# Kernel optimization log

Hardware: AMD Instinct MI355X
Metric: run time of the kernel (lower is better)

The kernel has to match this reference:

```python
import jax, jax.numpy as jnp
import numpy as np

N_TX = 1_000_000   # transaction nodes
N_W  = 250_000     # wallet nodes
E    = 2_000_000   # edges per relation
F_TX, F_W = 64, 32 # raw feature dims
H, OUT = 64, 2     # hidden, out (module defaults)


def setup_inputs() -> dict:
    key = jax.random.key(0)
    ks = jax.random.split(key, 40)
    f32 = jnp.float32
    def w(i, shape):
        return jax.random.normal(ks[i], shape, dtype=f32) * 0.05
    inp = {}
    inp["x_tx"] = jax.random.normal(ks[0], (N_TX, F_TX), dtype=f32)
    inp["x_w"]  = jax.random.normal(ks[1], (N_W, F_W), dtype=f32)
    inp["src_tw"] = jax.random.randint(ks[2], (E,), 0, N_TX)
    inp["dst_tw"] = jax.random.randint(ks[3], (E,), 0, N_W)
    inp["src_wt"] = jax.random.randint(ks[4], (E,), 0, N_W)
    inp["dst_wt"] = jax.random.randint(ks[5], (E,), 0, N_TX)
    # lin_in per node type
    inp["Win_tx"], inp["bin_tx"] = w(6, (F_TX, H)), w(7, (H,))
    inp["Win_w"],  inp["bin_w"]  = w(8, (F_W, H)),  w(9, (H,))
    # conv1: SAGEConv per edge type (lin_l has bias, lin_r no bias)
    inp["Wl1_tw"], inp["bl1_tw"], inp["Wr1_tw"] = w(10, (H, H)), w(11, (H,)), w(12, (H, H))
    inp["Wl1_wt"], inp["bl1_wt"], inp["Wr1_wt"] = w(13, (H, H)), w(14, (H,)), w(15, (H, H))
    # conv2
    inp["Wl2_tw"], inp["bl2_tw"], inp["Wr2_tw"] = w(16, (H, H)), w(17, (H,)), w(18, (H, H))
    inp["Wl2_wt"], inp["bl2_wt"], inp["Wr2_wt"] = w(19, (H, H)), w(20, (H,)), w(21, (H, H))
    # tx head
    inp["Wh1"], inp["bh1"] = w(22, (H, H)), w(23, (H,))
    inp["Wh2"], inp["bh2"] = w(24, (H, OUT)), w(25, (OUT,))
    return inp


def _sage(x_src, x_dst, src, dst, Wl, bl, Wr, n_dst):
    # PyG SAGEConv: lin_l(mean_{j->i} x_src[j]) + lin_r(x_dst[i])
    agg = jax.ops.segment_sum(x_src[src], dst, num_segments=n_dst)
    cnt = jax.ops.segment_sum(jnp.ones((src.shape[0],), x_src.dtype), dst,
                              num_segments=n_dst)
    mean = agg / jnp.maximum(cnt, 1.0)[:, None]
    return mean @ Wl + bl + x_dst @ Wr


def reference(x_tx, x_w, src_tw, dst_tw, src_wt, dst_wt,
              Win_tx, bin_tx, Win_w, bin_w,
              Wl1_tw, bl1_tw, Wr1_tw, Wl1_wt, bl1_wt, Wr1_wt,
              Wl2_tw, bl2_tw, Wr2_tw, Wl2_wt, bl2_wt, Wr2_wt,
              Wh1, bh1, Wh2, bh2):
    # per-type input projection
    h_tx = x_tx @ Win_tx + bin_tx   # [N_TX, H]
    h_w  = x_w @ Win_w + bin_w      # [N_W, H]
    # conv1 (HeteroConv aggr='sum'; each dst type has one relation) + relu
    w1 = jax.nn.relu(_sage(h_tx, h_w,  src_tw, dst_tw, Wl1_tw, bl1_tw, Wr1_tw, N_W))
    t1 = jax.nn.relu(_sage(h_w,  h_tx, src_wt, dst_wt, Wl1_wt, bl1_wt, Wr1_wt, N_TX))
    # conv2 + relu
    w2 = jax.nn.relu(_sage(t1, w1, src_tw, dst_tw, Wl2_tw, bl2_tw, Wr2_tw, N_W))
    t2 = jax.nn.relu(_sage(w1, t1, src_wt, dst_wt, Wl2_wt, bl2_wt, Wr2_wt, N_TX))
    # tx head (dropout inactive in eval)
    logits = jax.nn.relu(t2 @ Wh1 + bh1) @ Wh2 + bh2  # [N_TX, 2]
    return (logits, t2, w2)
```

## Files before the change

### kernel.cpp

```cpp
#include <hip/hip_runtime.h>
#include <hip/hip_bf16.h>

typedef __hip_bfloat16 bf16;
typedef __attribute__((ext_vector_type(8))) short bf16x8;
typedef __attribute__((ext_vector_type(4))) float f32x4;

__device__ __forceinline__ float b2f(bf16 v) { return __bfloat162float(v); }
__device__ __forceinline__ bf16 f2b(float v) { return __float2bfloat16(v); }
__device__ __forceinline__ unsigned short f2bb(float v) {
    unsigned int u = __float_as_uint(v);
    u += 0x7fffu + ((u >> 16) & 1u);
    return (unsigned short)(u >> 16);
}
__device__ __forceinline__ float b2fx(bf16x8 v, int k) {
    return __uint_as_float(((unsigned int)(unsigned short)v[k]) << 16);
}

__device__ __forceinline__ f32x4 mfma16(bf16x8 a, bf16x8 b, f32x4 c) {
    return __builtin_amdgcn_mfma_f32_16x16x32_bf16(a, b, c, 0, 0, 0);
}

__device__ __forceinline__ bf16x8 load_bfrag(const float* __restrict__ W, int k0, int col) {
    bf16x8 f;
#pragma unroll
    for (int j = 0; j < 8; ++j)
        f[j] = (short)f2bb(W[(size_t)(k0 + j) * 64 + col]);
    return f;
}

__device__ __forceinline__ int swzH(int row, int b) {
    return row * 128 + (b ^ ((row & 7) << 4));
}

__global__ void count_rank2_kernel(const int* __restrict__ dst_tw, int* __restrict__ deg_w,
                                   int* __restrict__ rank_tw, int ne_tw,
                                   const int* __restrict__ dst_wt, int* __restrict__ deg_tx,
                                   int* __restrict__ rank_wt, int ne_wt) {
    int e = blockIdx.x * 256 + threadIdx.x;
    if (e < ne_tw) rank_tw[e] = atomicAdd(&deg_w[dst_tw[e]], 1);
    else {
        int e2 = e - ne_tw;
        if (e2 < ne_wt) rank_wt[e2] = atomicAdd(&deg_tx[dst_wt[e2]], 1);
    }
}

__global__ void scan1m_kernel(const int* __restrict__ dw, int* __restrict__ ew,
                              int* __restrict__ pw, int nw, int npw,
                              const int* __restrict__ dt, int* __restrict__ et,
                              int* __restrict__ pt, int nt) {
    __shared__ int sT[256];
    const int* deg; int* excl; int* partial; int n; int b;
    if ((int)blockIdx.x < npw) { deg = dw; excl = ew; partial = pw; n = nw; b = blockIdx.x; }
    else { deg = dt; excl = et; partial = pt; n = nt; b = blockIdx.x - npw; }
    int tid = threadIdx.x;
    int base = b * 1024 + tid * 4;
    int v0 = (base + 0 < n) ? deg[base + 0] : 0;
    int v1 = (base + 1 < n) ? deg[base + 1] : 0;
    int v2 = (base + 2 < n) ? deg[base + 2] : 0;
    int v3 = (base + 3 < n) ? deg[base + 3] : 0;
    int t = v0 + v1 + v2 + v3;
    sT[tid] = t;
    __syncthreads();
    for (int off = 1; off < 256; off <<= 1) {
        int x = (tid >= off) ? sT[tid - off] : 0;
        __syncthreads();
        sT[tid] += x;
        __syncthreads();
    }
    int et2 = sT[tid] - t;
    if (tid == 255) partial[b] = sT[255];
    if (base + 0 < n) excl[base + 0] = et2;
    if (base + 1 < n) excl[base + 1] = et2 + v0;
    if (base + 2 < n) excl[base + 2] = et2 + v0 + v1;
    if (base + 3 < n) excl[base + 3] = et2 + v0 + v1 + v2;
}

__global__ void scan2m_kernel(int* __restrict__ pw, int npw, int* __restrict__ pt, int npt) {
    __shared__ int sT[256];
    __shared__ int carry;
    int* partial = blockIdx.x ? pt : pw;
    int np = blockIdx.x ? npt : npw;
    int tid = threadIdx.x;
    if (tid == 0) carry = 0;
    __syncthreads();
    for (int c = 0; c < np; c += 256) {
        int i = c + tid;
        int v = (i < np) ? partial[i] : 0;
        sT[tid] = v;
        __syncthreads();
        for (int off = 1; off < 256; off <<= 1) {
            int x = (tid >= off) ? sT[tid - off] : 0;
            __syncthreads();
            sT[tid] += x;
            __syncthreads();
        }
        int incl = sT[tid];
        int total = sT[255];
        if (i < np) partial[i] = carry + incl - v;
        __syncthreads();
        if (tid == 0) carry += total;
        __syncthreads();
    }
}

__global__ void scan3m_kernel(const int* __restrict__ ew, const int* __restrict__ pw,
                              int* __restrict__ rw, int nw, int nbw,
                              const int* __restrict__ et, const int* __restrict__ pt,
                              int* __restrict__ rt, int nt) {
    int b = blockIdx.x;
    const int* excl; const int* partial; int* rp; int n; int i;
    if (b < nbw) { i = b * 256 + threadIdx.x; excl = ew; partial = pw; rp = rw; n = nw; }
    else { i = (b - nbw) * 256 + threadIdx.x; excl = et; partial = pt; rp = rt; n = nt; }
    if (i < n) rp[i] = excl[i] + partial[i >> 10];
}

__device__ __forceinline__ void proj64_body(const float* __restrict__ x,
                                            const float* __restrict__ W,
                                            const float* __restrict__ b,
                                            bf16* __restrict__ out, int n, int bid) {
    int tid = threadIdx.x;
    int lane = tid & 63, w = tid >> 6;
    int lm = lane & 15, lq = lane >> 4;

    bf16x8 wc[4][2];
    float bv[4];
#pragma unroll
    for (int ct = 0; ct < 4; ++ct) {
        int colc = ct * 16 + lm;
        wc[ct][0] = load_bfrag(W, lq * 8, colc);
        wc[ct][1] = load_bfrag(W, 32 + lq * 8, colc);
        bv[ct] = b[colc];
    }

    int larow = w * 16 + lm;
    int row0 = bid * 512;
    if (row0 >= n) return;
    int ar = row0 + larow; ar = (ar < n) ? ar : (n - 1);
    const float* xrow = x + ((size_t)ar << 6);
    float4 p0 = *(const float4*)(xrow + lq * 8);
    float4 p1 = *(const float4*)(xrow + lq * 8 + 4);
    float4 p2 = *(const float4*)(xrow + 32 + lq * 8);
    float4 p3 = *(const float4*)(xrow + 32 + lq * 8 + 4);

    for (int g = 0; g < 8; ++g) {
        int gr0 = row0 + g * 64;
        if (gr0 >= n) break;
        float4 q0 = p0, q1 = p1, q2 = p2, q3 = p3;
        if (g < 7) {
            int nr = gr0 + 64 + larow; nr = (nr < n) ? nr : (n - 1);
            const float* nx = x + ((size_t)nr << 6);
            q0 = *(const float4*)(nx + lq * 8);
            q1 = *(const float4*)(nx + lq * 8 + 4);
            q2 = *(const float4*)(nx + 32 + lq * 8);
            q3 = *(const float4*)(nx + 32 + lq * 8 + 4);
        }
        bf16x8 a0, a1;
        a0[0] = (short)f2bb(p0.x); a0[1] = (short)f2bb(p0.y);
        a0[2] = (short)f2bb(p0.z); a0[3] = (short)f2bb(p0.w);
        a0[4] = (short)f2bb(p1.x); a0[5] = (short)f2bb(p1.y);
        a0[6] = (short)f2bb(p1.z); a0[7] = (short)f2bb(p1.w);
        a1[0] = (short)f2bb(p2.x); a1[1] = (short)f2bb(p2.y);
        a1[2] = (short)f2bb(p2.z); a1[3] = (short)f2bb(p2.w);
        a1[4] = (short)f2bb(p3.x); a1[5] = (short)f2bb(p3.y);
        a1[6] = (short)f2bb(p3.z); a1[7] = (short)f2bb(p3.w);
#pragma unroll
        for (int ct = 0; ct < 4; ++ct) {
            f32x4 acc = {0.f, 0.f, 0.f, 0.f};
            acc = mfma16(a0, wc[ct][0], acc);
            acc = mfma16(a1, wc[ct][1], acc);
            int colc = ct * 16 + lm;
#pragma unroll
            for (int r = 0; r < 4; ++r) {
                int grow = gr0 + w * 16 + lq * 4 + r;
                if (grow < n)
                    out[(size_t)grow * 64 + colc] = f2b(acc[r] + bv[ct]);
            }
        }
        p0 = q0; p1 = q1; p2 = q2; p3 = q3;
    }
}

__device__ __forceinline__ void proj32_body(const float* __restrict__ x,
                                            const float* __restrict__ W,
                                            const float* __restrict__ b,
                                            bf16* __restrict__ out, int n, int bid,
                                            float (*sW)[64], float* sb, float (*sx)[32]) {
    const int F = 32;
    int tid = threadIdx.x;
    for (int idx = tid; idx < F * 16; idx += 256)
        ((float4*)sW)[idx] = ((const float4*)W)[idx];
    if (tid < 64) sb[tid] = b[tid];
    int base = bid * 64;
    int w = tid >> 6, j = tid & 63;
    int lw = w * 4;
    for (int g = 0; g < 4; ++g) {
        int row0 = base + g * 16;
        __syncthreads();
        for (int idx = tid; idx < 4 * F; idx += 256) {
            int rr = idx / (F / 4), c4 = idx - rr * (F / 4);
            int row = row0 + rr;
            float4 v = (row < n) ? ((const float4*)x)[(size_t)row * (F / 4) + c4]
                                 : make_float4(0.f, 0.f, 0.f, 0.f);
            *(float4*)&sx[rr][c4 * 4] = v;
        }
        __syncthreads();
        float a0 = sb[j], a1 = sb[j], a2 = sb[j], a3 = sb[j];
#pragma unroll 2
        for (int k = 0; k < F; k += 4) {
            float w0 = sW[k][j], w1 = sW[k + 1][j], w2 = sW[k + 2][j], w3 = sW[k + 3][j];
            float4 m0 = *(const float4*)&sx[lw + 0][k];
            float4 m1 = *(const float4*)&sx[lw + 1][k];
            float4 m2 = *(const float4*)&sx[lw + 2][k];
            float4 m3 = *(const float4*)&sx[lw + 3][k];
            a0 += m0.x * w0 + m0.y * w1 + m0.z * w2 + m0.w * w3;
            a1 += m1.x * w0 + m1.y * w1 + m1.z * w2 + m1.w * w3;
            a2 += m2.x * w0 + m2.y * w1 + m2.z * w2 + m2.w * w3;
            a3 += m3.x * w0 + m3.y * w1 + m3.z * w2 + m3.w * w3;
        }
        int r0 = row0 + lw;
        if (r0 + 0 < n) out[(size_t)(r0 + 0) * 64 + j] = f2b(a0);
        if (r0 + 1 < n) out[(size_t)(r0 + 1) * 64 + j] = f2b(a1);
        if (r0 + 2 < n) out[(size_t)(r0 + 2) * 64 + j] = f2b(a2);
        if (r0 + 3 < n) out[(size_t)(r0 + 3) * 64 + j] = f2b(a3);
    }
}

__global__ __launch_bounds__(256)
void fused_front_kernel(const int* __restrict__ src_tw, const int* __restrict__ dst_tw,
                        const int* __restrict__ rank_tw, const int* __restrict__ rp_w,
                        int* __restrict__ col_tw, int ne_tw,
                        const int* __restrict__ src_wt, const int* __restrict__ dst_wt,
                        const int* __restrict__ rank_wt, const int* __restrict__ rp_tx,
                        int* __restrict__ col_wt, int ne_wt, int gsc,
                        const float* __restrict__ x_tx, const float* __restrict__ Win_tx,
                        const float* __restrict__ bin_tx, bf16* __restrict__ A, int n_tx, int gp64,
                        const float* __restrict__ x_w, const float* __restrict__ Win_w,
                        const float* __restrict__ bin_w, bf16* __restrict__ B, int n_w) {
    __shared__ float sW32[32][64];
    __shared__ float sb32[64];
    __shared__ float sx32[16][32];
    int bid = blockIdx.x;
    if (bid < gsc) {
        int e = bid * 256 + threadIdx.x;
        if (e < ne_tw) {
            col_tw[rp_w[dst_tw[e]] + rank_tw[e]] = src_tw[e];
        } else {
            int e2 = e - ne_tw;
            if (e2 < ne_wt)
                col_wt[rp_tx[dst_wt[e2]] + rank_wt[e2]] = src_wt[e2];
        }
    } else if (bid < gsc + gp64) {
        proj64_body(x_tx, Win_tx, bin_tx, A, n_tx, bid - gsc);
    } else {
        proj32_body(x_w, Win_w, bin_w, B, n_w, bid - gsc - gp64, sW32, sb32, sx32);
    }
}

#define GA4(x, wt) \
    p0 += (wt) * b2fx(x, 0); p1 += (wt) * b2fx(x, 1); \
    p2 += (wt) * b2fx(x, 2); p3 += (wt) * b2fx(x, 3); \
    p4 += (wt) * b2fx(x, 4); p5 += (wt) * b2fx(x, 5); \
    p6 += (wt) * b2fx(x, 6); p7 += (wt) * b2fx(x, 7);
#define GB4(x, wt) \
    q0 += (wt) * b2fx(x, 0); q1 += (wt) * b2fx(x, 1); \
    q2 += (wt) * b2fx(x, 2); q3 += (wt) * b2fx(x, 3); \
    q4 += (wt) * b2fx(x, 4); q5 += (wt) * b2fx(x, 5); \
    q6 += (wt) * b2fx(x, 6); q7 += (wt) * b2fx(x, 7);

template<bool HEAD>
__device__ __forceinline__ void sageg_body(
        const bf16* __restrict__ hsrc, const int* __restrict__ rowptr,
        const int* __restrict__ deg, const int* __restrict__ col,
        const bf16* __restrict__ xd,
        const float* __restrict__ Wl, const float* __restrict__ bl,
        const float* __restrict__ Wr,
        float* __restrict__ outf, bf16* __restrict__ outb,
        const float* __restrict__ Wh1, const float* __restrict__ bh1,
        const float* __restrict__ Wh2, const float* __restrict__ bh2,
        float* __restrict__ logits, int n, int bid, short* sH) {
    int tid = threadIdx.x;
    int lane = tid & 63, w = tid >> 6;
    int lm = lane & 15, lq = lane >> 4;

    bf16x8 wc[4][4];
    bf16x8 wh[4][2];
    float blv[4], h1v[4], w2a[4], w2b[4];
#pragma unroll
    for (int ct = 0; ct < 4; ++ct) {
        int colc = ct * 16 + lm;
        wc[ct][0] = load_bfrag(Wl, lq * 8, colc);
        wc[ct][1] = load_bfrag(Wl, 32 + lq * 8, colc);
        wc[ct][2] = load_bfrag(Wr, lq * 8, colc);
        wc[ct][3] = load_bfrag(Wr, 32 + lq * 8, colc);
        blv[ct] = bl[colc];
        if (HEAD) {
            wh[ct][0] = load_bfrag(Wh1, lq * 8, colc);
            wh[ct][1] = load_bfrag(Wh1, 32 + lq * 8, colc);
            h1v[ct] = bh1[colc];
            w2a[ct] = Wh2[colc * 2 + 0];
            w2b[ct] = Wh2[colc * 2 + 1];
        }
    }
    float b20 = 0.f, b21 = 0.f;
    if (HEAD) { b20 = bh2[0]; b21 = bh2[1]; }

    int larow = w * 16 + lm;
    int row0 = bid * 512;
    if (row0 >= n) return;
    int fo1 = lq * 8, fo2 = 32 + lq * 8;

    for (int g = 0; g < 8; ++g) {
        int gr0 = row0 + g * 64;
        if (gr0 >= n) break;
        int arow = gr0 + larow;
        int ar = (arow < n) ? arow : (n - 1);
        const bf16* xrow = xd + ((size_t)ar << 6);
        bf16x8 a2 = *(const bf16x8*)(xrow + fo1);
        bf16x8 a3 = *(const bf16x8*)(xrow + fo2);
        int base = rowptr[ar];
        int d = deg[ar];
        int lasto = (d > 0) ? d - 1 : 0;
        float p0 = 0.f, p1 = 0.f, p2 = 0.f, p3 = 0.f;
        float p4 = 0.f, p5 = 0.f, p6 = 0.f, p7 = 0.f;
        float q0 = 0.f, q1 = 0.f, q2 = 0.f, q3 = 0.f;
        float q4 = 0.f, q5 = 0.f, q6 = 0.f, q7 = 0.f;
        for (int e0 = 0; e0 < d; e0 += 4) {
            int o1 = (e0 + 1 < d) ? e0 + 1 : lasto;
            int o2 = (e0 + 2 < d) ? e0 + 2 : lasto;
            int o3 = (e0 + 3 < d) ? e0 + 3 : lasto;
            int s0 = col[base + e0], s1 = col[base + o1];
            int s2 = col[base + o2], s3 = col[base + o3];
            const bf16* r0p = hsrc + ((size_t)s0 << 6);
            const bf16* r1p = hsrc + ((size_t)s1 << 6);
            const bf16* r2p = hsrc + ((size_t)s2 << 6);
            const bf16* r3p = hsrc + ((size_t)s3 << 6);
            bf16x8 xa0 = *(const bf16x8*)(r0p + fo1);
            bf16x8 xb0 = *(const bf16x8*)(r0p + fo2);
            bf16x8 xa1 = *(const bf16x8*)(r1p + fo1);
            bf16x8 xb1 = *(const bf16x8*)(r1p + fo2);
            bf16x8 xa2 = *(const bf16x8*)(r2p + fo1);
            bf16x8 xb2 = *(const bf16x8*)(r2p + fo2);
            bf16x8 xa3 = *(const bf16x8*)(r3p + fo1);
            bf16x8 xb3 = *(const bf16x8*)(r3p + fo2);
            float w1 = (e0 + 1 < d) ? 1.f : 0.f;
            float w2 = (e0 + 2 < d) ? 1.f : 0.f;
            float w3 = (e0 + 3 < d) ? 1.f : 0.f;
            GA4(xa0, 1.f) GB4(xb0, 1.f)
            GA4(xa1, w1)  GB4(xb1, w1)
            GA4(xa2, w2)  GB4(xb2, w2)
            GA4(xa3, w3)  GB4(xb3, w3)
        }
        float dd = fmaxf((float)d, 1.f);
        bf16x8 a0, a1;
        a0[0] = (short)f2bb(p0 / dd); a0[1] = (short)f2bb(p1 / dd);
        a0[2] = (short)f2bb(p2 / dd); a0[3] = (short)f2bb(p3 / dd);
        a0[4] = (short)f2bb(p4 / dd); a0[5] = (short)f2bb(p5 / dd);
        a0[6] = (short)f2bb(p6 / dd); a0[7] = (short)f2bb(p7 / dd);
        a1[0] = (short)f2bb(q0 / dd); a1[1] = (short)f2bb(q1 / dd);
        a1[2] = (short)f2bb(q2 / dd); a1[3] = (short)f2bb(q3 / dd);
        a1[4] = (short)f2bb(q4 / dd); a1[5] = (short)f2bb(q5 / dd);
        a1[6] = (short)f2bb(q6 / dd); a1[7] = (short)f2bb(q7 / dd);

#pragma unroll
        for (int ct = 0; ct < 4; ++ct) {
            f32x4 acc = {0.f, 0.f, 0.f, 0.f};
            acc = mfma16(a0, wc[ct][0], acc);
            acc = mfma16(a1, wc[ct][1], acc);
            acc = mfma16(a2, wc[ct][2], acc);
            acc = mfma16(a3, wc[ct][3], acc);
            int colc = ct * 16 + lm;
#pragma unroll
            for (int r = 0; r < 4; ++r) {
                int lrow = w * 16 + lq * 4 + r;
                int grow = gr0 + lrow;
                float v = fmaxf(acc[r] + blv[ct], 0.f);
                if (grow < n) {
                    if (outf) outf[(size_t)grow * 64 + colc] = v;
                    if (outb) outb[(size_t)grow * 64 + colc] = f2b(v);
                }
                if (HEAD)
                    *(short*)((char*)sH + swzH(lrow, colc * 2)) = (short)f2bb(v);
            }
        }
        if (HEAD) {
            bf16x8 h0 = *(const bf16x8*)((char*)sH + swzH(larow, lq * 16));
            bf16x8 h1 = *(const bf16x8*)((char*)sH + swzH(larow, 64 + lq * 16));
            float qa0 = 0.f, qa1 = 0.f, qa2 = 0.f, qa3 = 0.f;
            float qb0 = 0.f, qb1 = 0.f, qb2 = 0.f, qb3 = 0.f;
#pragma unroll
            for (int ct = 0; ct < 4; ++ct) {
                f32x4 acc = {0.f, 0.f, 0.f, 0.f};
                acc = mfma16(h0, wh[ct][0], acc);
                acc = mfma16(h1, wh[ct][1], acc);
                float hb = h1v[ct];
                float h_0 = fmaxf(acc[0] + hb, 0.f);
                float h_1 = fmaxf(acc[1] + hb, 0.f);
                float h_2 = fmaxf(acc[2] + hb, 0.f);
                float h_3 = fmaxf(acc[3] + hb, 0.f);
                qa0 += h_0 * w2a[ct]; qb0 += h_0 * w2b[ct];
                qa1 += h_1 * w2a[ct]; qb1 += h_1 * w2b[ct];
                qa2 += h_2 * w2a[ct]; qb2 += h_2 * w2b[ct];
                qa3 += h_3 * w2a[ct]; qb3 += h_3 * w2b[ct];
            }
#pragma unroll
            for (int m = 8; m; m >>= 1) {
                qa0 += __shfl_xor(qa0, m); qb0 += __shfl_xor(qb0, m);
                qa1 += __shfl_xor(qa1, m); qb1 += __shfl_xor(qb1, m);
                qa2 += __shfl_xor(qa2, m); qb2 += __shfl_xor(qb2, m);
                qa3 += __shfl_xor(qa3, m); qb3 += __shfl_xor(qb3, m);
            }
            int rowb = gr0 + w * 16 + lq * 4;
            if (lm == 0) {
                if (rowb + 0 < n) { logits[(size_t)(rowb + 0) * 2 + 0] = qa0 + b20;
                                    logits[(size_t)(rowb + 0) * 2 + 1] = qb0 + b21; }
                if (rowb + 1 < n) { logits[(size_t)(rowb + 1) * 2 + 0] = qa1 + b20;
                                    logits[(size_t)(rowb + 1) * 2 + 1] = qb1 + b21; }
                if (rowb + 2 < n) { logits[(size_t)(rowb + 2) * 2 + 0] = qa2 + b20;
                                    logits[(size_t)(rowb + 2) * 2 + 1] = qb2 + b21; }
                if (rowb + 3 < n) { logits[(size_t)(rowb + 3) * 2 + 0] = qa3 + b20;
                                    logits[(size_t)(rowb + 3) * 2 + 1] = qb3 + b21; }
            }
        }
    }
}

template<bool HEAD>
__global__ __launch_bounds__(256)
void sageg2_kernel(const bf16* __restrict__ hw, const int* __restrict__ rpw,
                   const int* __restrict__ dgw, const int* __restrict__ clw,
                   const bf16* __restrict__ xw,
                   const float* __restrict__ Wlw, const float* __restrict__ blw,
                   const float* __restrict__ Wrw,
                   float* __restrict__ outfw, bf16* __restrict__ outbw, int nw, int gbw,
                   const bf16* __restrict__ ht, const int* __restrict__ rpt,
                   const int* __restrict__ dgt, const int* __restrict__ clt,
                   const bf16* __restrict__ xt,
                   const float* __restrict__ Wlt, const float* __restrict__ blt,
                   const float* __restrict__ Wrt,
                   float* __restrict__ outft, bf16* __restrict__ outbt,
                   const float* __restrict__ Wh1, const float* __restrict__ bh1,
                   const float* __restrict__ Wh2, const float* __restrict__ bh2,
                   float* __restrict__ logits, int nt) {
    __shared__ __align__(16) short sH[HEAD ? 64 * 64 : 8];
    if ((int)blockIdx.x < gbw)
        sageg_body<false>(hw, rpw, dgw, clw, xw, Wlw, blw, Wrw, outfw, outbw,
                          nullptr, nullptr, nullptr, nullptr, nullptr, nw, blockIdx.x, sH);
    else
        sageg_body<HEAD>(ht, rpt, dgt, clt, xt, Wlt, blt, Wrt, outft, outbt,
                         Wh1, bh1, Wh2, bh2, logits, nt, blockIdx.x - gbw, sH);
}

extern "C" void kernel_launch(void* const* d_in, const int* in_sizes, int n_in,
                              void* d_out, int out_size, void* d_ws, size_t ws_size,
                              hipStream_t stream) {
    const float* x_tx   = (const float*)d_in[0];
    const float* x_w    = (const float*)d_in[1];
    const int*   src_tw = (const int*)d_in[2];
    const int*   dst_tw = (const int*)d_in[3];
    const int*   src_wt = (const int*)d_in[4];
    const int*   dst_wt = (const int*)d_in[5];
    const float* Win_tx = (const float*)d_in[6];
    const float* bin_tx = (const float*)d_in[7];
    const float* Win_w  = (const float*)d_in[8];
    const float* bin_w  = (const float*)d_in[9];
    const float* Wl1_tw = (const float*)d_in[10];
    const float* bl1_tw = (const float*)d_in[11];
    const float* Wr1_tw = (const float*)d_in[12];
    const float* Wl1_wt = (const float*)d_in[13];
    const float* bl1_wt = (const float*)d_in[14];
    const float* Wr1_wt = (const float*)d_in[15];
    const float* Wl2_tw = (const float*)d_in[16];
    const float* bl2_tw = (const float*)d_in[17];
    const float* Wr2_tw = (const float*)d_in[18];
    const float* Wl2_wt = (const float*)d_in[19];
    const float* bl2_wt = (const float*)d_in[20];
    const float* Wr2_wt = (const float*)d_in[21];
    const float* Wh1    = (const float*)d_in[22];
    const float* bh1    = (const float*)d_in[23];
    const float* Wh2    = (const float*)d_in[24];
    const float* bh2    = (const float*)d_in[25];

    const int n_tx  = in_sizes[0] / 64;
    const int n_w   = in_sizes[1] / 32;
    const int ne_tw = in_sizes[2];
    const int ne_wt = in_sizes[4];

    bf16* A2      = (bf16*)d_ws;
    bf16* B2      = A2 + (size_t)n_tx * 64;
    bf16* A       = B2 + (size_t)n_w * 64;
    bf16* B       = A + (size_t)n_tx * 64;
    int*  deg_w   = (int*)(B + (size_t)n_w * 64);
    int*  deg_tx  = deg_w + n_w;
    int*  rp_w    = deg_tx + n_tx;
    int*  rp_tx   = rp_w + n_w;
    int*  ex_w    = rp_tx + n_tx;
    int*  ex_tx   = ex_w + n_w;
    int*  col_tw  = ex_tx + n_tx;
    int*  col_wt  = col_tw + ne_tw;
    int*  rank_tw = col_wt + ne_wt;
    int*  rank_wt = rank_tw + ne_tw;
    int*  part_w  = rank_wt + ne_wt;
    int*  part_tx = part_w + 4096;

    float* out_logits = (float*)d_out;
    float* out_t2 = out_logits + (size_t)n_tx * 2;
    float* out_w2 = out_t2 + (size_t)n_tx * 64;

    dim3 blk(256);
    int gp64 = (n_tx + 511) / 512;
    int gp32 = (n_w + 63) / 64;
    int gs_w  = (n_w + 511) / 512;
    int gs_tx = (n_tx + 511) / 512;
    int gsc = (ne_tw + ne_wt + 255) / 256;
    int np_w  = (n_w + 1023) / 1024;
    int np_tx = (n_tx + 1023) / 1024;
    int nbw = (n_w + 255) / 256;
    int nbt = (n_tx + 255) / 256;

    hipMemsetAsync(deg_w, 0, (size_t)n_w * sizeof(int), stream);
    hipMemsetAsync(deg_tx, 0, (size_t)n_tx * sizeof(int), stream);
    count_rank2_kernel<<<gsc, blk, 0, stream>>>(dst_tw, deg_w, rank_tw, ne_tw,
                                                dst_wt, deg_tx, rank_wt, ne_wt);
    scan1m_kernel<<<np_w + np_tx, blk, 0, stream>>>(deg_w, ex_w, part_w, n_w, np_w,
                                                    deg_tx, ex_tx, part_tx, n_tx);
    scan2m_kernel<<<2, blk, 0, stream>>>(part_w, np_w, part_tx, np_tx);
    scan3m_kernel<<<nbw + nbt, blk, 0, stream>>>(ex_w, part_w, rp_w, n_w, nbw,
                                                 ex_tx, part_tx, rp_tx, n_tx);

    fused_front_kernel<<<gsc + gp64 + gp32, blk, 0, stream>>>(
        src_tw, dst_tw, rank_tw, rp_w, col_tw, ne_tw,
        src_wt, dst_wt, rank_wt, rp_tx, col_wt, ne_wt, gsc,
        x_tx, Win_tx, bin_tx, A, n_tx, gp64,
        x_w, Win_w, bin_w, B, n_w);

    sageg2_kernel<false><<<gs_w + gs_tx, blk, 0, stream>>>(
        A, rp_w, deg_w, col_tw, B, Wl1_tw, bl1_tw, Wr1_tw, nullptr, B2, n_w, gs_w,
        B, rp_tx, deg_tx, col_wt, A, Wl1_wt, bl1_wt, Wr1_wt, nullptr, A2,
        nullptr, nullptr, nullptr, nullptr, nullptr, n_tx);

    sageg2_kernel<true><<<gs_w + gs_tx, blk, 0, stream>>>(
        A2, rp_w, deg_w, col_tw, B2, Wl2_tw, bl2_tw, Wr2_tw, out_w2, nullptr, n_w, gs_w,
        B2, rp_tx, deg_tx, col_wt, A2, Wl2_wt, bl2_wt, Wr2_wt, out_t2, nullptr,
        Wh1, bh1, Wh2, bh2, out_logits, n_tx);
}
```

Before: 1.342 ms.

## Prefetch next row metadata, stage bf16 outputs via LDS, two edges per thread

```diff
diff --git a/kernel.cpp b/kernel.cpp
--- a/kernel.cpp
+++ b/kernel.cpp
@@ -32,16 +32,24 @@
     return row * 128 + (b ^ ((row & 7) << 4));
 }
 
+__device__ __forceinline__ void cr_one(int e,
+        const int* __restrict__ dst_tw, int* __restrict__ deg_w,
+        int* __restrict__ rank_tw, int ne_tw,
+        const int* __restrict__ dst_wt, int* __restrict__ deg_tx,
+        int* __restrict__ rank_wt, int ne_wt) {
+    if (e < ne_tw) rank_tw[e] = atomicAdd(&deg_w[dst_tw[e]], 1);
+    else {
+        int e2 = e - ne_tw;
+        if (e2 < ne_wt) rank_wt[e2] = atomicAdd(&deg_tx[dst_wt[e2]], 1);
+    }
+}
 __global__ void count_rank2_kernel(const int* __restrict__ dst_tw, int* __restrict__ deg_w,
                                    int* __restrict__ rank_tw, int ne_tw,
                                    const int* __restrict__ dst_wt, int* __restrict__ deg_tx,
                                    int* __restrict__ rank_wt, int ne_wt) {
-    int e = blockIdx.x * 256 + threadIdx.x;
-    if (e < ne_tw) rank_tw[e] = atomicAdd(&deg_w[dst_tw[e]], 1);
-    else {
-        int e2 = e - ne_tw;
-        if (e2 < ne_wt) rank_wt[e2] = atomicAdd(&deg_tx[dst_wt[e2]], 1);
-    }
+    int t = blockIdx.x * 256 + threadIdx.x;
+    cr_one(t * 2 + 0, dst_tw, deg_w, rank_tw, ne_tw, dst_wt, deg_tx, rank_wt, ne_wt);
+    cr_one(t * 2 + 1, dst_tw, deg_w, rank_tw, ne_tw, dst_wt, deg_tx, rank_wt, ne_wt);
 }
 
 __global__ void scan1m_kernel(const int* __restrict__ dw, int* __restrict__ ew,
@@ -309,16 +317,24 @@
     if (row0 >= n) return;
     int fo1 = lq * 8, fo2 = 32 + lq * 8;
 
+    int ar0 = row0 + larow; ar0 = (ar0 < n) ? ar0 : (n - 1);
+    int base = rowptr[ar0];
+    int d = deg[ar0];
+
     for (int g = 0; g < 8; ++g) {
         int gr0 = row0 + g * 64;
         if (gr0 >= n) break;
         int arow = gr0 + larow;
         int ar = (arow < n) ? arow : (n - 1);
+        int nbase = base, nd = d;
+        if (g < 7) {
+            int nr = gr0 + 64 + larow; nr = (nr < n) ? nr : (n - 1);
+            nbase = rowptr[nr];
+            nd = deg[nr];
+        }
         const bf16* xrow = xd + ((size_t)ar << 6);
         bf16x8 a2 = *(const bf16x8*)(xrow + fo1);
         bf16x8 a3 = *(const bf16x8*)(xrow + fo2);
-        int base = rowptr[ar];
-        int d = deg[ar];
         int lasto = (d > 0) ? d - 1 : 0;
         float p0 = 0.f, p1 = 0.f, p2 = 0.f, p3 = 0.f;
         float p4 = 0.f, p5 = 0.f, p6 = 0.f, p7 = 0.f;
@@ -374,12 +390,17 @@
                 int lrow = w * 16 + lq * 4 + r;
                 int grow = gr0 + lrow;
                 float v = fmaxf(acc[r] + blv[ct], 0.f);
-                if (grow < n) {
-                    if (outf) outf[(size_t)grow * 64 + colc] = v;
-                    if (outb) outb[(size_t)grow * 64 + colc] = f2b(v);
-                }
-                if (HEAD)
+                if (outf && grow < n) outf[(size_t)grow * 64 + colc] = v;
+                if (outb || HEAD)
                     *(short*)((char*)sH + swzH(lrow, colc * 2)) = (short)f2bb(v);
+            }
+        }
+        if (outb) {
+            bf16x8 s0 = *(const bf16x8*)((char*)sH + swzH(larow, lq * 16));
+            bf16x8 s1 = *(const bf16x8*)((char*)sH + swzH(larow, 64 + lq * 16));
+            if (arow < n) {
+                *(bf16x8*)(outb + ((size_t)arow << 6) + fo1) = s0;
+                *(bf16x8*)(outb + ((size_t)arow << 6) + fo2) = s1;
             }
         }
         if (HEAD) {
@@ -421,6 +442,7 @@
                                     logits[(size_t)(rowb + 3) * 2 + 1] = qb3 + b21; }
             }
         }
+        base = nbase; d = nd;
     }
 }
 
@@ -441,7 +463,7 @@
                    const float* __restrict__ Wh1, const float* __restrict__ bh1,
                    const float* __restrict__ Wh2, const float* __restrict__ bh2,
                    float* __restrict__ logits, int nt) {
-    __shared__ __align__(16) short sH[HEAD ? 64 * 64 : 8];
+    __shared__ __align__(16) short sH[64 * 64];
     if ((int)blockIdx.x < gbw)
         sageg_body<false>(hw, rpw, dgw, clw, xw, Wlw, blw, Wrw, outfw, outbw,
                           nullptr, nullptr, nullptr, nullptr, nullptr, nw, blockIdx.x, sH);
@@ -512,6 +534,7 @@
     int gs_w  = (n_w + 511) / 512;
     int gs_tx = (n_tx + 511) / 512;
     int gsc = (ne_tw + ne_wt + 255) / 256;
+    int gcr = (ne_tw + ne_wt + 511) / 512;
     int np_w  = (n_w + 1023) / 1024;
     int np_tx = (n_tx + 1023) / 1024;
     int nbw = (n_w + 255) / 256;
@@ -519,7 +542,7 @@
 
     hipMemsetAsync(deg_w, 0, (size_t)n_w * sizeof(int), stream);
     hipMemsetAsync(deg_tx, 0, (size_t)n_tx * sizeof(int), stream);
-    count_rank2_kernel<<<gsc, blk, 0, stream>>>(dst_tw, deg_w, rank_tw, ne_tw,
+    count_rank2_kernel<<<gcr, blk, 0, stream>>>(dst_tw, deg_w, rank_tw, ne_tw,
                                                 dst_wt, deg_tx, rank_wt, ne_wt);
     scan1m_kernel<<<np_w + np_tx, blk, 0, stream>>>(deg_w, ex_w, part_w, n_w, np_w,
                                                     deg_tx, ex_tx, part_tx, n_tx);
```

Result: no change. 1.360 ms (+1.4%).
